# Optimization experiments

Measured on AMD Instinct MI355X. Metric: run time of the kernel, lower is better.

The kernel has to match this reference:

```python
import jax, jax.numpy as jnp
import numpy as np

C = 64          # channels
N = 4096        # number of sampled coords (64x64 grid)
SPACING = (0.001, 0.001)
SHIFT = jnp.array([SPACING[0] / 2.0, SPACING[1] / 2.0], dtype=jnp.float32)  # 'nearest' mode shift


def setup_inputs() -> dict:
    key = jax.random.key(0)
    k1, k2 = jax.random.split(key)
    values = jax.random.normal(k1, (C, N), dtype=jnp.float32)
    coords = jax.random.uniform(k2, (N, 2), dtype=jnp.float32)
    return {"values": values, "coords": coords}


def reference(values, coords):
    """upsample_nn, mode='nearest', grid_mode=True, scale=4.
    values: [C, N], coords: [N, 2] -> output [C, 4N]."""
    sx, sy = SPACING
    x, y = coords[:, 0], coords[:, 1]
    # three shifted copies of the grid -> [3N, 2]
    new_coords = jnp.concatenate([
        jnp.stack([x, y + sy], axis=1),
        jnp.stack([x + sx, y], axis=1),
        jnp.stack([x + sx, y + sy], axis=1),
    ], axis=0)
    q = new_coords - SHIFT                                  # [3N, 2]
    # squared pairwise distances via expansion (argmin-equivalent to norm)
    d2 = (q * q).sum(1)[:, None] + (coords * coords).sum(1)[None, :] \
         - 2.0 * (q @ coords.T)                             # [3N, N]
    idx = jnp.argmin(d2, axis=1)                            # nearest old coord per new coord
    new_values = values[:, idx]                             # [C, 3N] irregular gather
    return jnp.concatenate([values, new_values], axis=1)    # [C, 4N]
```

## Files before the change

kernel.cpp:

```cpp
#include <hip/hip_runtime.h>


#pragma clang fp contract(off)

constexpr int   Nn    = 4096;
constexpr int   Cc    = 64;
constexpr int   NQ    = 3 * Nn;
constexpr int   GD    = 32;
constexpr int   NCELL = GD * GD;
constexpr float Rm    = 3.5e-3f;
constexpr int   QPB   = 64;
constexpr int   QBLK  = NQ / QPB;

__global__ __launch_bounds__(256) void upsample_fused_kernel(
    const float* __restrict__ values,
    const float* __restrict__ coords,
    float* __restrict__ out)
{
#pragma clang fp contract(off)
    __shared__ int            sCnt[NCELL];
    __shared__ float2         sPts[Nn];
    __shared__ unsigned short sIds[Nn];
    __shared__ int            sBi[QPB];

    const int tid = threadIdx.x;

    for (int t = blockIdx.x * 256 + tid; t < Cc * (Nn / 4); t += QBLK * 256) {
        int row = t >> 10;
        int c4  = t & 1023;
        float4 v = reinterpret_cast<const float4*>(values)[row * 1024 + c4];
        reinterpret_cast<float4*>(out)[row * 4096 + c4] = v;
    }

    const int g    = tid >> 2;
    const int l    = tid & 3;
    const int q    = blockIdx.x * QPB + g;
    const int isrc = q & (Nn - 1);
    const float2 ci = reinterpret_cast<const float2*>(coords)[isrc];

    #pragma unroll
    for (int k = 0; k < NCELL / 256; ++k) sCnt[tid + 256 * k] = 0;

    float2 pt[16];
    int    cell[16];
    #pragma unroll
    for (int k = 0; k < 8; ++k) {
        int t4 = tid + 256 * k;
        float4 v = reinterpret_cast<const float4*>(coords)[t4];
        pt[2 * k]     = make_float2(v.x, v.y);
        pt[2 * k + 1] = make_float2(v.z, v.w);
    }
    __syncthreads();
    #pragma unroll
    for (int k = 0; k < 16; ++k) {
        int cx = min(GD - 1, (int)(pt[k].x * (float)GD));
        int cy = min(GD - 1, (int)(pt[k].y * (float)GD));
        cell[k] = cy * GD + cx;
        atomicAdd(&sCnt[cell[k]], 1);
    }
    __syncthreads();

    if (tid < 64) {
        int loc[16];
        int run = 0;
        #pragma unroll
        for (int k = 0; k < 16; ++k) { loc[k] = run; run += sCnt[tid * 16 + k]; }
        int inc = run;
        #pragma unroll
        for (int off = 1; off < 64; off <<= 1) {
            int nv = __shfl_up(inc, off, 64);
            if (tid >= off) inc += nv;
        }
        const int excl = inc - run;
        #pragma unroll
        for (int k = 0; k < 16; ++k) sCnt[tid * 16 + k] = excl + loc[k];
    }
    __syncthreads();

    #pragma unroll
    for (int k = 0; k < 16; ++k) {
        int pos = atomicAdd(&sCnt[cell[k]], 1);
        int j   = ((tid + 256 * (k >> 1)) << 1) | (k & 1);
        sPts[pos] = pt[k];
        sIds[pos] = (unsigned short)j;
    }
    __syncthreads();

    {
        const int var = q >> 12;
        const float x = ci.x, y = ci.y;
        float qx, qy;
        if (var == 0) {
            qx = x - 0.0005f;
            qy = (y + 0.001f) - 0.0005f;
        } else if (var == 1) {
            qx = (x + 0.001f) - 0.0005f;
            qy = y - 0.0005f;
        } else {
            qx = (x + 0.001f) - 0.0005f;
            qy = (y + 0.001f) - 0.0005f;
        }
        const float qq = qx * qx + qy * qy;

        const int xlo = max(0, (int)floorf((qx - Rm) * (float)GD));
        const int xhi = min(GD - 1, (int)floorf((qx + Rm) * (float)GD));
        const int ylo = max(0, (int)floorf((qy - Rm) * (float)GD));
        const int yhi = min(GD - 1, (int)floorf((qy + Rm) * (float)GD));

        float bd = INFINITY;
        int   bi = 0x7fffffff;
        for (int cy = ylo; cy <= yhi; ++cy) {
            int cellLo = cy * GD + xlo;
            int cellHi = cy * GD + xhi;
            int s = (cellLo == 0) ? 0 : sCnt[cellLo - 1];
            int e = sCnt[cellHi];
            for (int p = s + l; p < e; p += 4) {
                float2 c  = sPts[p];
                int    jj = sIds[p];
                float  cc = c.x * c.x + c.y * c.y;
                float  qc = __builtin_fmaf(qy, c.y, qx * c.x);
                float  d2 = (qq + cc) - (qc + qc);
                if (d2 < bd || (d2 == bd && jj < bi)) { bd = d2; bi = jj; }
            }
        }
        #pragma unroll
        for (int off = 1; off < 4; off <<= 1) {
            float od = __shfl_xor(bd, off, 64);
            int   oi = __shfl_xor(bi, off, 64);
            if (od < bd || (od == bd && oi < bi)) { bd = od; bi = oi; }
        }
        if (l == 0) sBi[g] = bi;
    }
    __syncthreads();

    {
        const int ql = tid & 63;
        const int cg = tid >> 6;
        const int bi = sBi[ql];
        const int q0 = blockIdx.x * QPB;
        #pragma unroll
        for (int k = 0; k < 16; ++k) {
            int ch = cg * 16 + k;
            out[(size_t)ch * (4 * Nn) + Nn + q0 + ql] = values[ch * Nn + bi];
        }
    }
}

extern "C" void kernel_launch(void* const* d_in, const int* in_sizes, int n_in,
                              void* d_out, int out_size, void* d_ws, size_t ws_size,
                              hipStream_t stream) {
    const float* values = (const float*)d_in[0];
    const float* coords = (const float*)d_in[1];
    float* out = (float*)d_out;
    hipLaunchKernelGGL(upsample_fused_kernel, dim3(QBLK), dim3(256), 0, stream,
                       values, coords, out);
}
```

Measured before the change: 10.92 us.

## Bucket only cells needed by block queries and overlap copy with search

Each block now first marks the grid cells its queries' search windows touch, then counts and scatters only the coordinate points that fall in marked cells. This cuts the shared-memory atomics and stores spent building the full 4096-point bucket in every block. Queries per block drop to 48 so the grid is 256 blocks, and the last wave copies the passthrough values while the first three waves do the nearest-neighbour search. The gather is re-indexed to cover 48 queries × 64 channels. The cost is an extra mark array, one more barrier, and a search that now uses only three of the four waves.

Result: slower. 11.95 us (+9.4%).

```diff
diff --git a/kernel.cpp b/kernel.cpp
--- a/kernel.cpp
+++ b/kernel.cpp
@@ -9,8 +9,8 @@
 constexpr int   GD    = 32;
 constexpr int   NCELL = GD * GD;
 constexpr float Rm    = 3.5e-3f;
-constexpr int   QPB   = 64;
-constexpr int   QBLK  = NQ / QPB;
+constexpr int   QPB   = 48;
+constexpr int   NBLK  = NQ / QPB;
 
 __global__ __launch_bounds__(256) void upsample_fused_kernel(
     const float* __restrict__ values,
@@ -19,18 +19,12 @@
 {
 #pragma clang fp contract(off)
     __shared__ int            sCnt[NCELL];
+    __shared__ int            sMark[NCELL];
     __shared__ float2         sPts[Nn];
     __shared__ unsigned short sIds[Nn];
     __shared__ int            sBi[QPB];
 
     const int tid = threadIdx.x;
-
-    for (int t = blockIdx.x * 256 + tid; t < Cc * (Nn / 4); t += QBLK * 256) {
-        int row = t >> 10;
-        int c4  = t & 1023;
-        float4 v = reinterpret_cast<const float4*>(values)[row * 1024 + c4];
-        reinterpret_cast<float4*>(out)[row * 4096 + c4] = v;
-    }
 
     const int g    = tid >> 2;
     const int l    = tid & 3;
@@ -38,9 +32,28 @@
     const int isrc = q & (Nn - 1);
     const float2 ci = reinterpret_cast<const float2*>(coords)[isrc];
 
+    const int var = q >> 12;
+    const float x = ci.x, y = ci.y;
+    float qx, qy;
+    if (var == 0) {
+        qx = x - 0.0005f;
+        qy = (y + 0.001f) - 0.0005f;
+    } else if (var == 1) {
+        qx = (x + 0.001f) - 0.0005f;
+        qy = y - 0.0005f;
+    } else {
+        qx = (x + 0.001f) - 0.0005f;
+        qy = (y + 0.001f) - 0.0005f;
+    }
+    const float qq = qx * qx + qy * qy;
+    const int xlo = max(0, (int)floorf((qx - Rm) * (float)GD));
+    const int xhi = min(GD - 1, (int)floorf((qx + Rm) * (float)GD));
+    const int ylo = max(0, (int)floorf((qy - Rm) * (float)GD));
+    const int yhi = min(GD - 1, (int)floorf((qy + Rm) * (float)GD));
+
     #pragma unroll
-    for (int k = 0; k < NCELL / 256; ++k) sCnt[tid + 256 * k] = 0;
-
+    for (int k = 0; k < NCELL / 256; ++k) { sCnt[tid + 256 * k] = 0;
+                                            sMark[tid + 256 * k] = 0; }
     float2 pt[16];
     int    cell[16];
     #pragma unroll
@@ -50,13 +63,25 @@
         pt[2 * k]     = make_float2(v.x, v.y);
         pt[2 * k + 1] = make_float2(v.z, v.w);
     }
-    __syncthreads();
     #pragma unroll
     for (int k = 0; k < 16; ++k) {
         int cx = min(GD - 1, (int)(pt[k].x * (float)GD));
         int cy = min(GD - 1, (int)(pt[k].y * (float)GD));
         cell[k] = cy * GD + cx;
-        atomicAdd(&sCnt[cell[k]], 1);
+    }
+    __syncthreads();
+
+    if (tid < 4 * QPB) {
+        int mx = min(xlo + (l & 1), xhi);
+        int my = min(ylo + (l >> 1), yhi);
+        sMark[my * GD + mx] = 1;
+    }
+    __syncthreads();
+
+    #pragma unroll
+    for (int k = 0; k < 16; ++k) {
+        if (sMark[cell[k]]) atomicAdd(&sCnt[cell[k]], 1);
+        else                cell[k] = -1;
     }
     __syncthreads();
 
@@ -79,34 +104,16 @@
 
     #pragma unroll
     for (int k = 0; k < 16; ++k) {
-        int pos = atomicAdd(&sCnt[cell[k]], 1);
-        int j   = ((tid + 256 * (k >> 1)) << 1) | (k & 1);
-        sPts[pos] = pt[k];
-        sIds[pos] = (unsigned short)j;
+        if (cell[k] >= 0) {
+            int pos = atomicAdd(&sCnt[cell[k]], 1);
+            int j   = ((tid + 256 * (k >> 1)) << 1) | (k & 1);
+            sPts[pos] = pt[k];
+            sIds[pos] = (unsigned short)j;
+        }
     }
     __syncthreads();
 
-    {
-        const int var = q >> 12;
-        const float x = ci.x, y = ci.y;
-        float qx, qy;
-        if (var == 0) {
-            qx = x - 0.0005f;
-            qy = (y + 0.001f) - 0.0005f;
-        } else if (var == 1) {
-            qx = (x + 0.001f) - 0.0005f;
-            qy = y - 0.0005f;
-        } else {
-            qx = (x + 0.001f) - 0.0005f;
-            qy = (y + 0.001f) - 0.0005f;
-        }
-        const float qq = qx * qx + qy * qy;
-
-        const int xlo = max(0, (int)floorf((qx - Rm) * (float)GD));
-        const int xhi = min(GD - 1, (int)floorf((qx + Rm) * (float)GD));
-        const int ylo = max(0, (int)floorf((qy - Rm) * (float)GD));
-        const int yhi = min(GD - 1, (int)floorf((qy + Rm) * (float)GD));
-
+    if (tid < 4 * QPB) {
         float bd = INFINITY;
         int   bi = 0x7fffffff;
         for (int cy = ylo; cy <= yhi; ++cy) {
@@ -130,17 +137,27 @@
             if (od < bd || (od == bd && oi < bi)) { bd = od; bi = oi; }
         }
         if (l == 0) sBi[g] = bi;
+    } else {
+        int t = tid - 192;
+        #pragma unroll
+        for (int k = 0; k < 4; ++k) {
+            int gi  = blockIdx.x * 256 + k * 64 + t;
+            int row = gi >> 10;
+            int c4  = gi & 1023;
+            float4 v = reinterpret_cast<const float4*>(values)[row * 1024 + c4];
+            reinterpret_cast<float4*>(out)[row * 4096 + c4] = v;
+        }
     }
     __syncthreads();
 
     {
-        const int ql = tid & 63;
-        const int cg = tid >> 6;
-        const int bi = sBi[ql];
         const int q0 = blockIdx.x * QPB;
         #pragma unroll
-        for (int k = 0; k < 16; ++k) {
-            int ch = cg * 16 + k;
+        for (int k = 0; k < 12; ++k) {
+            int idx = k * 256 + tid;
+            int ch  = idx / QPB;
+            int ql  = idx - ch * QPB;
+            int bi  = sBi[ql];
             out[(size_t)ch * (4 * Nn) + Nn + q0 + ql] = values[ch * Nn + bi];
         }
     }
@@ -152,6 +169,6 @@
     const float* values = (const float*)d_in[0];
     const float* coords = (const float*)d_in[1];
     float* out = (float*)d_out;
-    hipLaunchKernelGGL(upsample_fused_kernel, dim3(QBLK), dim3(256), 0, stream,
+    hipLaunchKernelGGL(upsample_fused_kernel, dim3(NBLK), dim3(256), 0, stream,
                        values, coords, out);
 }
```
